# Kernel tuning notes

Hardware: AMD Instinct MI355X
Metric: run time of the kernel (lower is better)

Reference implementation:

```python
import jax, jax.numpy as jnp
import numpy as np

N = 50000      # total nodes across batch of graphs
E = 800000     # total directed edges (avg degree 16)
B = 64         # number of graphs
D = 128        # input_dim == hidden_dim
L = 4          # num_layers - 1 GIN layers
OUT = 10
BN_EPS = 1e-5


def setup_inputs() -> dict:
    key = jax.random.key(0)
    ks = jax.random.split(key, 12)
    s = 0.05
    return {
        "x": jax.random.normal(ks[0], (N, D), jnp.float32),
        "pi": jax.random.uniform(ks[1], (B, 25), jnp.float32),
        "eps": jnp.zeros((L,), jnp.float32),
        "mlp_w1": jax.random.normal(ks[2], (L, D, D), jnp.float32) * s,
        "mlp_b1": jnp.zeros((L, D), jnp.float32),
        "mlp_bn_g": jnp.ones((L, D), jnp.float32),
        "mlp_bn_b": jnp.zeros((L, D), jnp.float32),
        "mlp_w2": jax.random.normal(ks[3], (L, D, D), jnp.float32) * s,
        "mlp_b2": jnp.zeros((L, D), jnp.float32),
        "bn_g": jnp.ones((L, D), jnp.float32),
        "bn_b": jnp.zeros((L, D), jnp.float32),
        "attend_w": jax.random.normal(ks[4], (D * (L + 1), 1), jnp.float32) * s,
        "attend_b": jnp.zeros((1,), jnp.float32),
        "pi_w": jax.random.normal(ks[5], (25, 16), jnp.float32) * s,
        "pi_b": jnp.zeros((16,), jnp.float32),
        "out_w": jax.random.normal(ks[6], (D * (L + 1) + 16, OUT), jnp.float32) * s,
        "out_b": jnp.zeros((OUT,), jnp.float32),
        "edge_index": jax.random.randint(ks[7], (2, E), 0, N, dtype=jnp.int32),
        "graph_id": jnp.sort(jax.random.randint(ks[8], (N,), 0, B, dtype=jnp.int32)),
    }


def _bn(z, g, b):
    # BatchNorm1d in training mode over all nodes (axis 0)
    m = z.mean(axis=0)
    v = z.var(axis=0)
    return (z - m) * jax.lax.rsqrt(v + BN_EPS) * g + b


def reference(x, pi, eps, mlp_w1, mlp_b1, mlp_bn_g, mlp_bn_b, mlp_w2, mlp_b2,
              bn_g, bn_b, attend_w, attend_b, pi_w, pi_b, out_w, out_b,
              edge_index, graph_id):
    src, dst = edge_index[0], edge_index[1]
    h = x
    reps = [x]
    for l in range(L):
        # GIN sum aggregation (learn_eps=True: no self-loops in Adj)
        pooled = jax.ops.segment_sum(h[src], dst, num_segments=N)
        pooled = pooled + (1.0 + eps[l]) * h
        # 2-layer MLP: Linear -> BN -> ReLU -> Linear
        z = jax.nn.relu(_bn(pooled @ mlp_w1[l] + mlp_b1[l], mlp_bn_g[l], mlp_bn_b[l]))
        z = z @ mlp_w2[l] + mlp_b2[l]
        # outer BN + ReLU
        h = jax.nn.relu(_bn(z, bn_g[l], bn_b[l]))
        reps.append(h)
    hr = jnp.concatenate(reps, axis=1)               # [N, D*(L+1)]
    # per-graph attention softmax over nodes
    scores = (hr @ attend_w + attend_b)[:, 0]        # [N]
    smax = jax.ops.segment_max(scores, graph_id, num_segments=B)
    e = jnp.exp(scores - smax[graph_id])
    denom = jax.ops.segment_sum(e, graph_id, num_segments=B)
    coef = e / denom[graph_id]
    gemb = jax.ops.segment_sum(hr * coef[:, None], graph_id, num_segments=B)  # [B, D*(L+1)]
    # persistence-image branch (PI computed host-side; treated as input)
    pie = jax.nn.relu(pi @ pi_w + pi_b)              # [B, 16]
    feat = jnp.concatenate([gemb, pie], axis=1)      # [B, D*(L+1)+16]
    return feat @ out_w + out_b                      # [B, OUT]
```

## Files before the change

kernel.cpp:

```cpp
#include <hip/hip_runtime.h>
#include <hip/hip_bf16.h>

#define NN 50000
#define EE 800000
#define BBG 64
#define DD 128
#define LLAY 4
#define HRW 640
#define NOUT 10
#define NXCD 8
#define NBUCK 196
#define BUCKCAP 4608
#define EB 250
#define ECH 3200

typedef __hip_bfloat16 bf16;
typedef __attribute__((ext_vector_type(8))) short short8;
typedef __attribute__((ext_vector_type(4))) float f32x4;

__device__ __forceinline__ float b2f(bf16 v) { return __bfloat162float(v); }
__device__ __forceinline__ float bflo(unsigned u) { return __uint_as_float(u << 16); }
__device__ __forceinline__ float bfhi(unsigned u) { return __uint_as_float(u & 0xffff0000u); }
__device__ __forceinline__ unsigned short f2bs(float v) {
  bf16 h = __float2bfloat16(v);
  unsigned short r; __builtin_memcpy(&r, &h, 2); return r;
}
__device__ __forceinline__ int dtype_of(const void* __restrict__ bng) {
  return (*(const unsigned*)bng == 0x3F800000u) ? 1 : 0;
}
__device__ __forceinline__ float ldf(const void* __restrict__ p, long i, int dt) {
  return dt ? ((const float*)p)[i] : b2f(((const bf16*)p)[i]);
}

__device__ __forceinline__ int xccid() {
  unsigned v;
  asm("s_getreg_b32 %0, hwreg(HW_REG_XCC_ID)" : "=s"(v));
  return (int)(v & (NXCD - 1));
}

__device__ __forceinline__ void fadd_l2(float* p, float v) {
  asm volatile("global_atomic_add_f32 %0, %1, off" :: "v"(p), "v"(v) : "memory");
}

__device__ __forceinline__ int lower_bound_i(const int* __restrict__ a, int n, int key) {
  int lo = 0, hi = n;
  while (lo < hi) { int mid = (lo + hi) >> 1; if (a[mid] < key) lo = mid + 1; else hi = mid; }
// ... 1 lines not shown
}

__global__ __launch_bounds__(256) void gnn_init(const void* __restrict__ x,
                                                bf16* __restrict__ hrb,
                                                const void* __restrict__ w1,
                                                const void* __restrict__ w2,
                                                bf16* __restrict__ w1t,
                                                bf16* __restrict__ w2t,
                                                const void* __restrict__ aw,
                                                float* __restrict__ scores,
                                                const int* __restrict__ ei,
                                                int* __restrict__ bucketCnt,
                                                unsigned* __restrict__ bucketStore,
                                                const void* __restrict__ bng) {
  int dt = dtype_of(bng);
  int tid = threadIdx.x;
  if (blockIdx.x >= 3375) {
    int i = (blockIdx.x - 3375) * 256 + tid;
    int l = i >> 14, rem = i & 16383, n = rem >> 7, k = rem & 127;
    long src = (long)l * 16384 + k * 128 + n;
    w1t[i] = __float2bfloat16(ldf(w1, src, dt));
    w2t[i] = __float2bfloat16(ldf(w2, src, dt));
    return;
  }
  if (blockIdx.x >= 3125) {
    __shared__ int lcnt[NBUCK], gbase[NBUCK];
    int bb = blockIdx.x - 3125;
    int base = bb * ECH;
    if (tid < NBUCK) lcnt[tid] = 0;
    __syncthreads();
    #pragma unroll
    for (int j = 0; j < 13; j++) {
      int k = j * 256 + tid;
      if (k < ECH) {
        int dst = ei[EE + base + k];
        atomicAdd(&lcnt[dst >> 8], 1);
      }
    }
    __syncthreads();
    if (tid < NBUCK) {
      gbase[tid] = atomicAdd(&bucketCnt[tid * 16], lcnt[tid]);
      lcnt[tid] = 0;
    }
    __syncthreads();
    #pragma unroll
    for (int j = 0; j < 13; j++) {
      int k = j * 256 + tid;
      if (k < ECH) {
        int e = base + k;
        int src = ei[e];
        int dst = ei[EE + e];
        int b = dst >> 8;
        int r = atomicAdd(&lcnt[b], 1);
        bucketStore[b * BUCKCAP + gbase[b] + r] =
            (unsigned)src | ((unsigned)(dst & 255) << 16);
      }
    }
    return;
  }
  int n = blockIdx.x * 16 + (tid >> 4);
  int il = tid & 15;
  long base = (long)n * DD + il * 8;
  float v[8];
  if (dt) {
    float4 a0 = *(const float4*)((const float*)x + base);
    float4 a1 = *(const float4*)((const float*)x + base + 4);
    v[0] = a0.x; v[1] = a0.y; v[2] = a0.z; v[3] = a0.w;
    v[4] = a1.x; v[5] = a1.y; v[6] = a1.z; v[7] = a1.w;
  } else {
    uint4 u = *(const uint4*)((const bf16*)x + base);
// ... 27 lines not shown
    if (tid < s) buf[tid] += buf[tid + s];
    __syncthreads();
  }
  int start = buf[0];
  int sz = bucketCnt[b * 16];
  __syncthreads();
  cnt[tid] = 0;
  __syncthreads();
  for (int j = 0; j < 18; j++) {
    int k = j * 256 + tid;
    if (k < sz) atomicAdd(&cnt[bucketStore[b * BUCKCAP + k] >> 16], 1);
  }
  __syncthreads();
  int c = cnt[tid];
  buf[tid] = c;
  __syncthreads();
  for (int ofs = 1; ofs < 256; ofs <<= 1) {
    int t = (tid >= ofs) ? buf[tid - ofs] : 0;
    __syncthreads();
    buf[tid] += t;
    __syncthreads();
  }
  dbase[tid] = buf[tid] - c;
  int d = b * 256 + tid;
  if (d <= NN) rowstart[d] = start + buf[tid] - c;
  cnt[tid] = 0;
  __syncthreads();
  for (int j = 0; j < 18; j++) {
    int k = j * 256 + tid;
    if (k < sz) {
      unsigned v = bucketStore[b * BUCKCAP + k];
      int dlo = v >> 16;
      int r = atomicAdd(&cnt[dlo], 1);
      csr_src[start + dbase[dlo] + r] = (int)(v & 0xFFFFu) | ((dlo & 15) << 16);
    }
  }
}

__device__ __forceinline__ float2 statsum(const float* __restrict__ stat, int c) {
  float s = 0.f, q = 0.f;
  #pragma unroll
  for (int k = 0; k < 8; k++) { s += stat[k * 256 + c]; q += stat[k * 256 + 128 + c]; }
  return make_float2(s, q);
}

__device__ __forceinline__ void acc8(float* a, uint4 u) {
  a[0] += bflo(u.x); a[1] += bfhi(u.x);
  a[2] += bflo(u.y); a[3] += bfhi(u.y);
  a[4] += bflo(u.z); a[5] += bfhi(u.z);
  a[6] += bflo(u.w); a[7] += bfhi(u.w);
}

__device__ __forceinline__ void ldg16(const bf16* __restrict__ stripe, int idx, int j,
                                      int q, int il,
                                      uint4& u0, uint4& u1, uint4& u2, uint4& u3) {
  int s0 = __shfl(idx, j + q, 64) & 0xFFFF;
  int s1 = __shfl(idx, j + 4 + q, 64) & 0xFFFF;
  int s2 = __shfl(idx, j + 8 + q, 64) & 0xFFFF;
  int s3 = __shfl(idx, j + 12 + q, 64) & 0xFFFF;
  u0 = *(const uint4*)(stripe + (size_t)s0 * HRW + il * 8);
  u1 = *(const uint4*)(stripe + (size_t)s1 * HRW + il * 8);
  u2 = *(const uint4*)(stripe + (size_t)s2 * HRW + il * 8);
  u3 = *(const uint4*)(stripe + (size_t)s3 * HRW + il * 8);
}

__global__ __launch_bounds__(256) void gnn_gmg1(const bf16* __restrict__ hrb, int l,
                                                const int* __restrict__ rowstart,
                                                const int* __restrict__ csr_src,
                                                const void* __restrict__ eps,
                                                const bf16* __restrict__ Wt,
                                                const void* __restrict__ bias, int biasOfs,
                                                bf16* __restrict__ out,
                                                float* __restrict__ statOut,
                                                const void* __restrict__ bng) {
  int dt = dtype_of(bng);
  __shared__ __align__(16) unsigned ar[16][68];
  __shared__ int rs[17];
  __shared__ int qhead;
  int tid = threadIdx.x, lane = tid & 63;
  int w = tid >> 6;
  int q = lane >> 4, il = lane & 15;
  int r0 = blockIdx.x * 16;
  const bf16* stripe = hrb + l * DD;
  float s = 1.0f + ldf(eps, l, dt);
  if (tid < 17) rs[tid] = rowstart[r0 + tid];
  if (tid == 0) qhead = 0;
  __syncthreads();

  int i, start = 0, end = 0, idx = 0;
  {
    int v;
    if (lane == 0) v = atomicAdd(&qhead, 1);
    i = __shfl(v, 0, 64);
    if (i < 16) {
      start = rs[i]; end = rs[i + 1];
      idx = (start + lane < end) ? csr_src[start + lane] : 0;
    }
  }
  while (i < 16) {
    int i_nxt;
    {
      int v;
      if (lane == 0) v = atomicAdd(&qhead, 1);
      i_nxt = __shfl(v, 0, 64);
    }
    int start_n = 0, end_n = 0, idx_n = 0;
    if (i_nxt < 16) {
      start_n = rs[i_nxt]; end_n = rs[i_nxt + 1];
      idx_n = (start_n + lane < end_n) ? csr_src[start_n + lane] : 0;
    }

    float a[8] = {0.f, 0.f, 0.f, 0.f, 0.f, 0.f, 0.f, 0.f};
    if (q == 0) {
      uint4 u = *(const uint4*)(stripe + (size_t)(r0 + i) * HRW + il * 8);
      a[0] = s * bflo(u.x); a[1] = s * bfhi(u.x);
      a[2] = s * bflo(u.y); a[3] = s * bfhi(u.y);
      a[4] = s * bflo(u.z); a[5] = s * bfhi(u.z);
      a[6] = s * bflo(u.w); a[7] = s * bfhi(u.w);
    }
    int p = start;
    int m = end - p; if (m > 64) m = 64;
    for (;;) {
      int j = 0;
      if (m >= 16) {
        uint4 c0, c1, c2, c3;
        ldg16(stripe, idx, 0, q, il, c0, c1, c2, c3);
        for (j = 16; j + 16 <= m; j += 16) {
          uint4 n0, n1, n2, n3;
          ldg16(stripe, idx, j, q, il, n0, n1, n2, n3);
          acc8(a, c0); acc8(a, c1); acc8(a, c2); acc8(a, c3);
          c0 = n0; c1 = n1; c2 = n2; c3 = n3;
        }
        acc8(a, c0); acc8(a, c1); acc8(a, c2); acc8(a, c3);
      }
      for (; j + 8 <= m; j += 8) {
        int s0 = __shfl(idx, j + q, 64) & 0xFFFF;
        int s1 = __shfl(idx, j + 4 + q, 64) & 0xFFFF;
        uint4 u0 = *(const uint4*)(stripe + (size_t)s0 * HRW + il * 8);
        uint4 u1 = *(const uint4*)(stripe + (size_t)s1 * HRW + il * 8);
        acc8(a, u0); acc8(a, u1);
      }
      for (; j + 4 <= m; j += 4) {
        int s0 = __shfl(idx, j + q, 64) & 0xFFFF;
        uint4 u0 = *(const uint4*)(stripe + (size_t)s0 * HRW + il * 8);
        acc8(a, u0);
      }
      for (; j < m; j++) {
        int s0 = __shfl(idx, j, 64) & 0xFFFF;
        if (q == 0) {
          uint4 u0 = *(const uint4*)(stripe + (size_t)s0 * HRW + il * 8);
          acc8(a, u0);
        }
      }
      p += m;
      if (p >= end) break;
      m = end - p; if (m > 64) m = 64;
      idx = (p + lane < end) ? csr_src[p + lane] : 0;
    }
    #pragma unroll
    for (int k = 0; k < 8; k++) {
      a[k] += __shfl_xor(a[k], 16, 64);
      a[k] += __shfl_xor(a[k], 32, 64);
    }
    if (q == 0) {
      uint4 o;
      o.x = (unsigned)f2bs(a[0]) | ((unsigned)f2bs(a[1]) << 16);
      o.y = (unsigned)f2bs(a[2]) | ((unsigned)f2bs(a[3]) << 16);
      o.z = (unsigned)f2bs(a[4]) | ((unsigned)f2bs(a[5]) << 16);
      o.w = (unsigned)f2bs(a[6]) | ((unsigned)f2bs(a[7]) << 16);
      *(uint4*)&ar[i][il * 4] = o;
    }
    i = i_nxt; start = start_n; end = end_n; idx = idx_n;
  }
  __syncthreads();

  int xid = xccid();
  #pragma unroll
  for (int t = 0; t < 2; t++) {
    int ct = w + t * 4;
    f32x4 acc = (f32x4){0.f, 0.f, 0.f, 0.f};
    #pragma unroll
    for (int ch = 0; ch < 4; ch++) {
      int k0 = ch * 32 + q * 8;
      uint4 raw2 = *(const uint4*)&ar[il][ch * 16 + q * 4];
      short8 af;
      __builtin_memcpy(&af, &raw2, 16);
      short8 bfv = *(const short8*)(Wt + (ct * 16 + il) * DD + k0);
      acc = __builtin_amdgcn_mfma_f32_16x16x32_bf16(af, bfv, acc, 0, 0, 0);
    }
    int col = ct * 16 + il;
    float bv = ldf(bias, biasOfs + col, dt);
    float ss = 0.f, qq = 0.f;
    #pragma unroll
    for (int r = 0; r < 4; r++) {
      int row = r0 + q * 4 + r;
      float v = acc[r] + bv;
      out[(size_t)row * DD + col] = __float2bfloat16(v);
      ss += v; qq += v * v;
    }
    ss += __shfl_xor(ss, 16, 64);  ss += __shfl_xor(ss, 32, 64);
    qq += __shfl_xor(qq, 16, 64);  qq += __shfl_xor(qq, 32, 64);
    if (q == 0) {
      fadd_l2(&statOut[xid * 256 + col], ss);
      fadd_l2(&statOut[xid * 256 + 128 + col], qq);
    }
  }
}

__global__ __launch_bounds__(256) void gnn_mgemm(const bf16* __restrict__ Abf,
                                                 const bf16* __restrict__ Wt,
                                                 const void* __restrict__ bias, int biasOfs,
                                                 bf16* __restrict__ out,
                                                 const float* __restrict__ statIn,
                                                 const void* __restrict__ g,
                                                 const void* __restrict__ bb, int parOfs,
                                                 float* __restrict__ statOut,
                                                 const void* __restrict__ bng) {
  int dt = dtype_of(bng);
  __shared__ float scf[128], shf[128];
  __shared__ float redS[4][128], redQ[4][128];
// ... 57 lines not shown
    if (q == 0) { redS[w][col] = s; redQ[w][col] = qq; }
  }
  __syncthreads();
  int xid = xccid();
  if (tid < 128) {
    float v = redS[0][tid] + redS[1][tid] + redS[2][tid] + redS[3][tid];
    fadd_l2(&statOut[xid * 256 + tid], v);
  } else {
    int c = tid - 128;
    float v = redQ[0][c] + redQ[1][c] + redQ[2][c] + redQ[3][c];
    fadd_l2(&statOut[xid * 256 + 128 + c], v);
  }
}

__global__ __launch_bounds__(256) void gnn_bn_relu(const bf16* __restrict__ z2,
                                                   const float* __restrict__ stat,
                                                   const void* __restrict__ g,
                                                   const void* __restrict__ bb, int parOfs,
                                                   bf16* __restrict__ hrb, int stripe,
                                                   const void* __restrict__ aw,
                                                   float* __restrict__ scores,
                                                   const void* __restrict__ bng) {
  int dt = dtype_of(bng);
  __shared__ float scf[128], shf[128], awf[128];
  int tid = threadIdx.x;
  if (tid < 128) {
    const float invN = 1.0f / NN;
    float2 sq = statsum(stat, tid);
    float m = sq.x * invN;
    float rs = rsqrtf(sq.y * invN - m * m + 1e-5f);
    float gg = ldf(g, parOfs + tid, dt), bv = ldf(bb, parOfs + tid, dt);
    scf[tid] = rs * gg;
    shf[tid] = bv - m * rs * gg;
    awf[tid] = ldf(aw, stripe * DD + tid, dt);
  }
  __syncthreads();
  int n = blockIdx.x * 16 + (tid >> 4);
  int il = tid & 15;
  int c0 = il * 8;
  uint4 u = *(const uint4*)(z2 + (size_t)n * DD + c0);
  float v[8];
  v[0] = bflo(u.x); v[1] = bfhi(u.x); v[2] = bflo(u.y); v[3] = bfhi(u.y);
  v[4] = bflo(u.z); v[5] = bfhi(u.z); v[6] = bflo(u.w); v[7] = bfhi(u.w);
  float ss = 0.f;
  #pragma unroll
  for (int k = 0; k < 8; k++) {
    v[k] = fmaxf(v[k] * scf[c0 + k] + shf[c0 + k], 0.f);
    ss += v[k] * awf[c0 + k];
  }
  uint4 o;
  o.x = (unsigned)f2bs(v[0]) | ((unsigned)f2bs(v[1]) << 16);
  o.y = (unsigned)f2bs(v[2]) | ((unsigned)f2bs(v[3]) << 16);
  o.z = (unsigned)f2bs(v[4]) | ((unsigned)f2bs(v[5]) << 16);
  o.w = (unsigned)f2bs(v[6]) | ((unsigned)f2bs(v[7]) << 16);
  *(uint4*)(hrb + (size_t)n * HRW + stripe * DD + c0) = o;
  ss += __shfl_xor(ss, 1, 64); ss += __shfl_xor(ss, 2, 64);
  ss += __shfl_xor(ss, 4, 64); ss += __shfl_xor(ss, 8, 64);
  if (il == 0) scores[n] += ss;
}

__global__ __launch_bounds__(128) void gnn_gemb(const bf16* __restrict__ hrb,
                                                const float* __restrict__ scores,
                                                const int* __restrict__ gid,
                                                float* __restrict__ gembp) {
  int b = blockIdx.x / 10;
  int part = blockIdx.x % 10;
  int chunk = part >> 1;
  int half = part & 1;
  int tid = threadIdx.x;
  int start = lower_bound_i(gid, NN, b);
  int end = lower_bound_i(gid, NN, b + 1);
  __shared__ float red[128];
  float mx = -3.4e38f;
  for (int n = start + tid; n < end; n += 128) mx = fmaxf(mx, scores[n]);
  red[tid] = mx;
  __syncthreads();
  for (int s = 64; s > 0; s >>= 1) {
    if (tid < s) red[tid] = fmaxf(red[tid], red[tid + s]);
    __syncthreads();
  }
  float smax = red[0];
  __syncthreads();
  float sum = 0.f;
  for (int n = start + tid; n < end; n += 128) sum += __expf(scores[n] - smax);
  red[tid] = sum;
  __syncthreads();
  for (int s = 64; s > 0; s >>= 1) {
    if (tid < s) red[tid] += red[tid + s];
// ... 81 lines not shown
  const void* bng  = d_in[5];
  const void* bnb  = d_in[6];
  const void* w2   = d_in[7];
  const void* b2   = d_in[8];
  const void* obng = d_in[9];
  const void* obnb = d_in[10];
  const void* aw   = d_in[11];
  const void* piw  = d_in[13];
  const void* pib  = d_in[14];
  const void* ow   = d_in[15];
  const void* ob   = d_in[16];
  const int*  ei   = (const int*)d_in[17];
  const int*  gid  = (const int*)d_in[18];

  bf16*  hrb      = (bf16*)d_ws;
  bf16*  z1       = hrb + (size_t)NN * HRW;
  bf16*  z2       = z1 + (size_t)NN * DD;
  bf16*  w1t      = z2 + (size_t)NN * DD;
  bf16*  w2t      = w1t + LLAY * DD * DD;
  float* statbufs = (float*)(w2t + LLAY * DD * DD);
  int*   bucketCnt= (int*)(statbufs + 8 * 2048);
  size_t zeroBytes = (size_t)(8 * 2048 + NBUCK * 16) * 4;
  float* gembp    = (float*)(bucketCnt + NBUCK * 16);
  float* scores   = gembp + (size_t)16 * BBG * HRW;
  int*   rowstart = (int*)(scores + NN);
  unsigned* bucketStore = (unsigned*)(rowstart + NN + 1);
  int*   csr_src  = (int*)(bucketStore + (size_t)NBUCK * BUCKCAP);

  hipMemsetAsync(statbufs, 0, zeroBytes, stream);
  gnn_init<<<3631, 256, 0, stream>>>(x, hrb, w1, w2, w1t, w2t, aw, scores,
                                     ei, bucketCnt, bucketStore, bng);
  gnn_csr<<<NBUCK, 256, 0, stream>>>(bucketCnt, bucketStore, rowstart, csr_src);

  for (int l = 0; l < LLAY; l++) {
    float* statA = statbufs + (l * 2 + 0) * 2048;
    float* statB = statbufs + (l * 2 + 1) * 2048;
    gnn_gmg1<<<NN / 16, 256, 0, stream>>>(hrb, l, rowstart, csr_src, eps,
                                          w1t + l * DD * DD, b1, l * DD,
                                          z1, statA, bng);
    gnn_mgemm<<<782, 256, 0, stream>>>(z1, w2t + l * DD * DD, b2, l * DD,
                                       z2, statA, bng, bnb, l * DD,
                                       statB, bng);
    gnn_bn_relu<<<NN / 16, 256, 0, stream>>>(z2, statB, obng, obnb, l * DD,
                                             hrb, l + 1, aw, scores, bng);
  }

  gnn_gemb<<<BBG * 10, 128, 0, stream>>>(hrb, scores, gid, gembp);
  gnn_final<<<BBG, 64, 0, stream>>>(gembp, pi, piw, pib, ow, ob, d_out, bng);
}
```

Before: 523.6 us.

## Fuse per-layer kernels into one cooperative persistent kernel with grid syncs

Replaces the 14 per-layer and readout kernel launches with a single cooperative persistent kernel. It uses grid.sync between the gather+GEMM1, GEMM2, BN/ReLU, attention-pooling and final stages, and loops over tiles with a grid sized from occupancy. The aim is to remove launch overhead and inter-kernel gaps. In exchange it adds grid-wide barrier costs, possibly lower occupancy from the 4-blocks-per-CU launch bound, and extra shared memory per block. The old multi-kernel path stays as a fallback.

```diff
diff --git a/kernel.cpp b/kernel.cpp
--- a/kernel.cpp
+++ b/kernel.cpp
@@ -1,5 +1,8 @@
 #include <hip/hip_runtime.h>
 #include <hip/hip_bf16.h>
+#include <hip/hip_cooperative_groups.h>
+
+namespace cg = cooperative_groups;
 
 #define NN 50000
 #define EE 800000
@@ -208,6 +211,390 @@
   u3 = *(const uint4*)(stripe + (size_t)s3 * HRW + il * 8);
 }
 
+__device__ __forceinline__ void gather_tile(const bf16* __restrict__ stripe,
+                                            const int* __restrict__ csr_src,
+                                            const int* rs, int* qhead_p,
+                                            unsigned (*ar)[68],
+                                            int r0, float s, int lane, int q, int il) {
+  int i, rstart = 0, rend = 0, idx = 0;
+  {
+    int v;
+    if (lane == 0) v = atomicAdd(qhead_p, 1);
+    i = __shfl(v, 0, 64);
+    if (i < 16) {
+      rstart = rs[i]; rend = rs[i + 1];
+      idx = (rstart + lane < rend) ? csr_src[rstart + lane] : 0;
+    }
+  }
+  while (i < 16) {
+    int i_nxt;
+    {
+      int v;
+      if (lane == 0) v = atomicAdd(qhead_p, 1);
+      i_nxt = __shfl(v, 0, 64);
+    }
+    int start_n = 0, end_n = 0, idx_n = 0;
+    if (i_nxt < 16) {
+      start_n = rs[i_nxt]; end_n = rs[i_nxt + 1];
+      idx_n = (start_n + lane < end_n) ? csr_src[start_n + lane] : 0;
+    }
+
+    float av[8] = {0.f, 0.f, 0.f, 0.f, 0.f, 0.f, 0.f, 0.f};
+    if (q == 0) {
+      uint4 u = *(const uint4*)(stripe + (size_t)(r0 + i) * HRW + il * 8);
+      av[0] = s * bflo(u.x); av[1] = s * bfhi(u.x);
+      av[2] = s * bflo(u.y); av[3] = s * bfhi(u.y);
+      av[4] = s * bflo(u.z); av[5] = s * bfhi(u.z);
+      av[6] = s * bflo(u.w); av[7] = s * bfhi(u.w);
+    }
+    int p = rstart;
+    int m = rend - p; if (m > 64) m = 64;
+    for (;;) {
+      int j = 0;
+      if (m >= 16) {
+        uint4 c0v, c1v, c2v, c3v;
+        ldg16(stripe, idx, 0, q, il, c0v, c1v, c2v, c3v);
+        for (j = 16; j + 16 <= m; j += 16) {
+          uint4 n0, n1, n2, n3;
+          ldg16(stripe, idx, j, q, il, n0, n1, n2, n3);
+          acc8(av, c0v); acc8(av, c1v); acc8(av, c2v); acc8(av, c3v);
+          c0v = n0; c1v = n1; c2v = n2; c3v = n3;
+        }
+        acc8(av, c0v); acc8(av, c1v); acc8(av, c2v); acc8(av, c3v);
+      }
+      for (; j + 8 <= m; j += 8) {
+        int s0 = __shfl(idx, j + q, 64) & 0xFFFF;
+        int s1 = __shfl(idx, j + 4 + q, 64) & 0xFFFF;
+        uint4 u0 = *(const uint4*)(stripe + (size_t)s0 * HRW + il * 8);
+        uint4 u1 = *(const uint4*)(stripe + (size_t)s1 * HRW + il * 8);
+        acc8(av, u0); acc8(av, u1);
+      }
+      for (; j + 4 <= m; j += 4) {
+        int s0 = __shfl(idx, j + q, 64) & 0xFFFF;
+        uint4 u0 = *(const uint4*)(stripe + (size_t)s0 * HRW + il * 8);
+        acc8(av, u0);
+      }
+      for (; j < m; j++) {
+        int s0 = __shfl(idx, j, 64) & 0xFFFF;
+        if (q == 0) {
+          uint4 u0 = *(const uint4*)(stripe + (size_t)s0 * HRW + il * 8);
+          acc8(av, u0);
+        }
+      }
+      p += m;
+      if (p >= rend) break;
+      m = rend - p; if (m > 64) m = 64;
+      idx = (p + lane < rend) ? csr_src[p + lane] : 0;
+    }
+    #pragma unroll
+    for (int k = 0; k < 8; k++) {
+      av[k] += __shfl_xor(av[k], 16, 64);
+      av[k] += __shfl_xor(av[k], 32, 64);
+    }
+    if (q == 0) {
+      uint4 o;
+      o.x = (unsigned)f2bs(av[0]) | ((unsigned)f2bs(av[1]) << 16);
+      o.y = (unsigned)f2bs(av[2]) | ((unsigned)f2bs(av[3]) << 16);
+      o.z = (unsigned)f2bs(av[4]) | ((unsigned)f2bs(av[5]) << 16);
+      o.w = (unsigned)f2bs(av[6]) | ((unsigned)f2bs(av[7]) << 16);
+      *(uint4*)&ar[i][il * 4] = o;
+    }
+    i = i_nxt; rstart = start_n; rend = end_n; idx = idx_n;
+  }
+}
+
+struct MegaArgs {
+  bf16* hrb;
+  const int* rowstart;
+  const int* csr_src;
+  const void* eps;
+  const bf16* w1t;
+  const bf16* w2t;
+  const void* b1;
+  const void* b2;
+  const void* bng;
+  const void* bnb;
+  const void* obng;
+  const void* obnb;
+  const void* aw;
+  float* scores;
+  bf16* z1;
+  bf16* z2;
+  float* statbufs;
+  float* gembp;
+  const int* gid;
+  const void* pi;
+  const void* piw;
+  const void* pib;
+  const void* ow;
+  const void* ob;
+  void* out;
+};
+
+__global__ __launch_bounds__(256, 4) void gnn_mega(MegaArgs a) {
+  cg::grid_group grid = cg::this_grid();
+  int dt = dtype_of(a.bng);
+  int tid = threadIdx.x, lane = tid & 63, w = tid >> 6;
+  int q = lane >> 4, il = lane & 15;
+  int xid = xccid();
+
+  __shared__ __align__(16) unsigned ar[16][68];
+  __shared__ int rs[17];
+  __shared__ int qhead;
+  __shared__ float scf[128], shf[128], awf[128];
+  __shared__ float redS[4][128], redQ[4][128];
+  __shared__ float red[2][128];
+
+  for (int l = 0; l < LLAY; l++) {
+    float* statA = a.statbufs + (l * 2 + 0) * 2048;
+    float* statB = a.statbufs + (l * 2 + 1) * 2048;
+    const bf16* stripe = a.hrb + l * DD;
+    const bf16* Wt1 = a.w1t + l * DD * DD;
+    const bf16* Wt2 = a.w2t + l * DD * DD;
+    float s = 1.0f + ldf(a.eps, l, dt);
+
+    for (int tile = blockIdx.x; tile < NN / 16; tile += gridDim.x) {
+      int r0 = tile * 16;
+      if (tid < 17) rs[tid] = a.rowstart[r0 + tid];
+      if (tid == 0) qhead = 0;
+      __syncthreads();
+      gather_tile(stripe, a.csr_src, rs, &qhead, ar, r0, s, lane, q, il);
+      __syncthreads();
+      #pragma unroll
+      for (int t2 = 0; t2 < 2; t2++) {
+        int ct = w + t2 * 4;
+        f32x4 macc = (f32x4){0.f, 0.f, 0.f, 0.f};
+        #pragma unroll
+        for (int ch = 0; ch < 4; ch++) {
+          uint4 raw2 = *(const uint4*)&ar[il][ch * 16 + q * 4];
+          short8 af;
+          __builtin_memcpy(&af, &raw2, 16);
+          short8 bfv = *(const short8*)(Wt1 + (ct * 16 + il) * DD + ch * 32 + q * 8);
+          macc = __builtin_amdgcn_mfma_f32_16x16x32_bf16(af, bfv, macc, 0, 0, 0);
+        }
+        int col = ct * 16 + il;
+        float bv = ldf(a.b1, l * DD + col, dt);
+        float ss = 0.f, qq = 0.f;
+        #pragma unroll
+        for (int r = 0; r < 4; r++) {
+          int row = r0 + q * 4 + r;
+          float v = macc[r] + bv;
+          a.z1[(size_t)row * DD + col] = __float2bfloat16(v);
+          ss += v; qq += v * v;
+        }
+        ss += __shfl_xor(ss, 16, 64);  ss += __shfl_xor(ss, 32, 64);
+        qq += __shfl_xor(qq, 16, 64);  qq += __shfl_xor(qq, 32, 64);
+        if (q == 0) {
+          fadd_l2(&statA[xid * 256 + col], ss);
+          fadd_l2(&statA[xid * 256 + 128 + col], qq);
+        }
+      }
+      __syncthreads();
+    }
+    grid.sync();
+
+    if (tid < 128) {
+      const float invN = 1.0f / NN;
+      float2 sq = statsum(statA, tid);
+      float m = sq.x * invN;
+      float rsi = rsqrtf(sq.y * invN - m * m + 1e-5f);
+      float gg = ldf(a.bng, l * DD + tid, dt), bv = ldf(a.bnb, l * DD + tid, dt);
+      scf[tid] = rsi * gg;
+      shf[tid] = bv - m * rsi * gg;
+    }
+    __syncthreads();
+    for (int tile = blockIdx.x; tile < 782; tile += gridDim.x) {
+      int r0b = (tile * 4 + w) * 16;
+      int arow = r0b + il;
+      int arowc = (arow < NN) ? arow : (NN - 1);
+      f32x4 acc[8];
+      #pragma unroll
+      for (int i = 0; i < 8; i++) acc[i] = (f32x4){0.f, 0.f, 0.f, 0.f};
+      #pragma unroll
+      for (int ch = 0; ch < 4; ch++) {
+        int k0 = ch * 32 + q * 8;
+        uint4 raw = *(const uint4*)(a.z1 + (size_t)arowc * DD + k0);
+        float4 c0 = *(const float4*)(scf + k0);
+        float4 c1 = *(const float4*)(scf + k0 + 4);
+        float4 d0 = *(const float4*)(shf + k0);
+        float4 d1 = *(const float4*)(shf + k0 + 4);
+        short8 af;
+        af[0] = (short)f2bs(fmaxf(bflo(raw.x) * c0.x + d0.x, 0.f));
+        af[1] = (short)f2bs(fmaxf(bfhi(raw.x) * c0.y + d0.y, 0.f));
+        af[2] = (short)f2bs(fmaxf(bflo(raw.y) * c0.z + d0.z, 0.f));
+        af[3] = (short)f2bs(fmaxf(bfhi(raw.y) * c0.w + d0.w, 0.f));
+        af[4] = (short)f2bs(fmaxf(bflo(raw.z) * c1.x + d1.x, 0.f));
+        af[5] = (short)f2bs(fmaxf(bfhi(raw.z) * c1.y + d1.y, 0.f));
+        af[6] = (short)f2bs(fmaxf(bflo(raw.w) * c1.z + d1.z, 0.f));
+        af[7] = (short)f2bs(fmaxf(bfhi(raw.w) * c1.w + d1.w, 0.f));
+        #pragma unroll
+        for (int ct = 0; ct < 8; ct++) {
+          short8 bfv = *(const short8*)(Wt2 + (ct * 16 + il) * DD + k0);
+          acc[ct] = __builtin_amdgcn_mfma_f32_16x16x32_bf16(af, bfv, acc[ct], 0, 0, 0);
+        }
+      }
+      #pragma unroll
+      for (int ct = 0; ct < 8; ct++) {
+        int col = ct * 16 + il;
+        float bv = ldf(a.b2, l * DD + col, dt);
+        float sv = 0.f, qq = 0.f;
+        #pragma unroll
+        for (int r = 0; r < 4; r++) {
+          int row = r0b + q * 4 + r;
+          float v = acc[ct][r] + bv;
+          if (row < NN) {
+            a.z2[(size_t)row * DD + col] = __float2bfloat16(v);
+            sv += v; qq += v * v;
+          }
+        }
+        sv += __shfl_xor(sv, 16, 64);  sv += __shfl_xor(sv, 32, 64);
+        qq += __shfl_xor(qq, 16, 64);  qq += __shfl_xor(qq, 32, 64);
+        if (q == 0) { redS[w][col] = sv; redQ[w][col] = qq; }
+      }
+      __syncthreads();
+      if (tid < 128) {
+        float v = redS[0][tid] + redS[1][tid] + redS[2][tid] + redS[3][tid];
+        fadd_l2(&statB[xid * 256 + tid], v);
+      } else {
+        int c = tid - 128;
+        float v = redQ[0][c] + redQ[1][c] + redQ[2][c] + redQ[3][c];
+        fadd_l2(&statB[xid * 256 + 128 + c], v);
+      }
+      __syncthreads();
+    }
+    grid.sync();
+
+    if (tid < 128) {
+      const float invN = 1.0f / NN;
+      float2 sq = statsum(statB, tid);
+      float m = sq.x * invN;
+      float rsi = rsqrtf(sq.y * invN - m * m + 1e-5f);
+      float gg = ldf(a.obng, l * DD + tid, dt), bv = ldf(a.obnb, l * DD + tid, dt);
+      scf[tid] = rsi * gg;
+      shf[tid] = bv - m * rsi * gg;
+      awf[tid] = ldf(a.aw, (l + 1) * DD + tid, dt);
+    }
+    __syncthreads();
+    for (int tile = blockIdx.x; tile < NN / 16; tile += gridDim.x) {
+      int n = tile * 16 + (tid >> 4);
+      int c0 = il * 8;
+      uint4 u = *(const uint4*)(a.z2 + (size_t)n * DD + c0);
+      float v[8];
+      v[0] = bflo(u.x); v[1] = bfhi(u.x); v[2] = bflo(u.y); v[3] = bfhi(u.y);
+      v[4] = bflo(u.z); v[5] = bfhi(u.z); v[6] = bflo(u.w); v[7] = bfhi(u.w);
+      float ss = 0.f;
+      #pragma unroll
+      for (int k = 0; k < 8; k++) {
+        v[k] = fmaxf(v[k] * scf[c0 + k] + shf[c0 + k], 0.f);
+        ss += v[k] * awf[c0 + k];
+      }
+      uint4 o;
+      o.x = (unsigned)f2bs(v[0]) | ((unsigned)f2bs(v[1]) << 16);
+      o.y = (unsigned)f2bs(v[2]) | ((unsigned)f2bs(v[3]) << 16);
+      o.z = (unsigned)f2bs(v[4]) | ((unsigned)f2bs(v[5]) << 16);
+      o.w = (unsigned)f2bs(v[6]) | ((unsigned)f2bs(v[7]) << 16);
+      *(uint4*)(a.hrb + (size_t)n * HRW + (l + 1) * DD + c0) = o;
+      ss += __shfl_xor(ss, 1, 64); ss += __shfl_xor(ss, 2, 64);
+      ss += __shfl_xor(ss, 4, 64); ss += __shfl_xor(ss, 8, 64);
+      if (il == 0) a.scores[n] += ss;
+    }
+    grid.sync();
+  }
+
+  for (int pb = blockIdx.x; pb < 320; pb += gridDim.x) {
+    __syncthreads();
+    int t = tid & 127, hid = tid >> 7;
+    int part = pb * 2 + hid;
+    int b = part / 10;
+    int sub = part % 10;
+    int chunk = sub >> 1;
+    int shalf = sub & 1;
+    int start = lower_bound_i(a.gid, NN, b);
+    int end = lower_bound_i(a.gid, NN, b + 1);
+    float mx = -3.4e38f;
+    for (int n = start + t; n < end; n += 128) mx = fmaxf(mx, a.scores[n]);
+    red[hid][t] = mx;
+    __syncthreads();
+    for (int s = 64; s > 0; s >>= 1) {
+      if (t < s) red[hid][t] = fmaxf(red[hid][t], red[hid][t + s]);
+      __syncthreads();
+    }
+    float smax = red[hid][0];
+    __syncthreads();
+    float sum = 0.f;
+    for (int n = start + t; n < end; n += 128) sum += __expf(a.scores[n] - smax);
+    red[hid][t] = sum;
+    __syncthreads();
+    for (int s = 64; s > 0; s >>= 1) {
+      if (t < s) red[hid][t] += red[hid][t + s];
+      __syncthreads();
+    }
+    float denom = red[hid][0];
+    float inv = (denom > 0.f) ? 1.0f / denom : 0.f;
+    int cg2 = t & 15;
+    int sl = shalf * 8 + (t >> 4);
+    int c0 = chunk * 128 + cg2 * 8;
+    float acc[8] = {0.f, 0.f, 0.f, 0.f, 0.f, 0.f, 0.f, 0.f};
+    for (int n = start + sl; n < end; n += 16) {
+      float wgt = __expf(a.scores[n] - smax) * inv;
+      uint4 u = *(const uint4*)(a.hrb + (size_t)n * HRW + c0);
+      acc[0] = fmaf(bflo(u.x), wgt, acc[0]);
+      acc[1] = fmaf(bfhi(u.x), wgt, acc[1]);
+      acc[2] = fmaf(bflo(u.y), wgt, acc[2]);
+      acc[3] = fmaf(bfhi(u.y), wgt, acc[3]);
+      acc[4] = fmaf(bflo(u.z), wgt, acc[4]);
+      acc[5] = fmaf(bfhi(u.z), wgt, acc[5]);
+      acc[6] = fmaf(bflo(u.w), wgt, acc[6]);
+      acc[7] = fmaf(bfhi(u.w), wgt, acc[7]);
+    }
+    float* dst = a.gembp + ((size_t)sl * BBG + b) * HRW + c0;
+    *(float4*)dst = make_float4(acc[0], acc[1], acc[2], acc[3]);
+    *(float4*)(dst + 4) = make_float4(acc[4], acc[5], acc[6], acc[7]);
+  }
+  grid.sync();
+
+  for (int b = blockIdx.x; b < BBG; b += gridDim.x) {
+    if (tid < 64) {
+      int t = tid;
+      float pieval = 0.f;
+      if (t < 16) {
+        float sv = ldf(a.pib, t, dt);
+        for (int i = 0; i < 25; i++)
+          sv += ldf(a.pi, b * 25 + i, dt) * ldf(a.piw, i * 16 + t, dt);
+        pieval = fmaxf(sv, 0.f);
+      }
+      float fv[11];
+      #pragma unroll
+      for (int i = 0; i < 11; i++) {
+        int c = t + i * 64;
+        float f = 0.f;
+        if (c < HRW) {
+          #pragma unroll
+          for (int s2 = 0; s2 < 16; s2++) f += a.gembp[((size_t)s2 * BBG + b) * HRW + c];
+        } else if (c < HRW + 16) {
+          f = pieval;
+        }
+        fv[i] = f;
+      }
+      for (int o = 0; o < NOUT; o++) {
+        float sv = 0.f;
+        #pragma unroll
+        for (int i = 0; i < 11; i++) {
+          int c = t + i * 64;
+          if (c < HRW + 16) sv += fv[i] * ldf(a.ow, (long)c * NOUT + o, dt);
+        }
+        #pragma unroll
+        for (int m = 32; m > 0; m >>= 1) sv += __shfl_xor(sv, m, 64);
+        if (t == 0) {
+          float r = sv + ldf(a.ob, o, dt);
+          if (dt) ((float*)a.out)[b * NOUT + o] = r;
+          else ((bf16*)a.out)[b * NOUT + o] = __float2bfloat16(r);
+        }
+      }
+    }
+  }
+}
+
 __global__ __launch_bounds__(256) void gnn_gmg1(const bf16* __restrict__ hrb, int l,
                                                 const int* __restrict__ rowstart,
                                                 const int* __restrict__ csr_src,
@@ -230,94 +617,8 @@
   if (tid < 17) rs[tid] = rowstart[r0 + tid];
   if (tid == 0) qhead = 0;
   __syncthreads();
-
-  int i, start = 0, end = 0, idx = 0;
-  {
-    int v;
-    if (lane == 0) v = atomicAdd(&qhead, 1);
-    i = __shfl(v, 0, 64);
-    if (i < 16) {
-      start = rs[i]; end = rs[i + 1];
-      idx = (start + lane < end) ? csr_src[start + lane] : 0;
-    }
-  }
-  while (i < 16) {
-    int i_nxt;
-    {
-      int v;
-      if (lane == 0) v = atomicAdd(&qhead, 1);
-      i_nxt = __shfl(v, 0, 64);
-    }
-    int start_n = 0, end_n = 0, idx_n = 0;
-    if (i_nxt < 16) {
-      start_n = rs[i_nxt]; end_n = rs[i_nxt + 1];
-      idx_n = (start_n + lane < end_n) ? csr_src[start_n + lane] : 0;
-    }
-
-    float a[8] = {0.f, 0.f, 0.f, 0.f, 0.f, 0.f, 0.f, 0.f};
-    if (q == 0) {
-      uint4 u = *(const uint4*)(stripe + (size_t)(r0 + i) * HRW + il * 8);
-      a[0] = s * bflo(u.x); a[1] = s * bfhi(u.x);
-      a[2] = s * bflo(u.y); a[3] = s * bfhi(u.y);
-      a[4] = s * bflo(u.z); a[5] = s * bfhi(u.z);
-      a[6] = s * bflo(u.w); a[7] = s * bfhi(u.w);
-    }
-    int p = start;
-    int m = end - p; if (m > 64) m = 64;
-    for (;;) {
-      int j = 0;
-      if (m >= 16) {
-        uint4 c0, c1, c2, c3;
-        ldg16(stripe, idx, 0, q, il, c0, c1, c2, c3);
-        for (j = 16; j + 16 <= m; j += 16) {
-          uint4 n0, n1, n2, n3;
-          ldg16(stripe, idx, j, q, il, n0, n1, n2, n3);
-          acc8(a, c0); acc8(a, c1); acc8(a, c2); acc8(a, c3);
-          c0 = n0; c1 = n1; c2 = n2; c3 = n3;
-        }
-        acc8(a, c0); acc8(a, c1); acc8(a, c2); acc8(a, c3);
-      }
-      for (; j + 8 <= m; j += 8) {
-        int s0 = __shfl(idx, j + q, 64) & 0xFFFF;
-        int s1 = __shfl(idx, j + 4 + q, 64) & 0xFFFF;
-        uint4 u0 = *(const uint4*)(stripe + (size_t)s0 * HRW + il * 8);
-        uint4 u1 = *(const uint4*)(stripe + (size_t)s1 * HRW + il * 8);
-        acc8(a, u0); acc8(a, u1);
-      }
-      for (; j + 4 <= m; j += 4) {
-        int s0 = __shfl(idx, j + q, 64) & 0xFFFF;
-        uint4 u0 = *(const uint4*)(stripe + (size_t)s0 * HRW + il * 8);
-        acc8(a, u0);
-      }
-      for (; j < m; j++) {
-        int s0 = __shfl(idx, j, 64) & 0xFFFF;
-        if (q == 0) {
-          uint4 u0 = *(const uint4*)(stripe + (size_t)s0 * HRW + il * 8);
-          acc8(a, u0);
-        }
-      }
-      p += m;
-      if (p >= end) break;
-      m = end - p; if (m > 64) m = 64;
-      idx = (p + lane < end) ? csr_src[p + lane] : 0;
-    }
-    #pragma unroll
-    for (int k = 0; k < 8; k++) {
-      a[k] += __shfl_xor(a[k], 16, 64);
-      a[k] += __shfl_xor(a[k], 32, 64);
-    }
-    if (q == 0) {
-      uint4 o;
-      o.x = (unsigned)f2bs(a[0]) | ((unsigned)f2bs(a[1]) << 16);
-      o.y = (unsigned)f2bs(a[2]) | ((unsigned)f2bs(a[3]) << 16);
-      o.z = (unsigned)f2bs(a[4]) | ((unsigned)f2bs(a[5]) << 16);
-      o.w = (unsigned)f2bs(a[6]) | ((unsigned)f2bs(a[7]) << 16);
-      *(uint4*)&ar[i][il * 4] = o;
-    }
-    i = i_nxt; start = start_n; end = end_n; idx = idx_n;
-  }
-  __syncthreads();
-
+  gather_tile(stripe, csr_src, rs, &qhead, ar, r0, s, lane, q, il);
+  __syncthreads();
   int xid = xccid();
   #pragma unroll
   for (int t = 0; t < 2; t++) {
@@ -325,11 +626,10 @@
     f32x4 acc = (f32x4){0.f, 0.f, 0.f, 0.f};
     #pragma unroll
     for (int ch = 0; ch < 4; ch++) {
-      int k0 = ch * 32 + q * 8;
       uint4 raw2 = *(const uint4*)&ar[il][ch * 16 + q * 4];
       short8 af;
       __builtin_memcpy(&af, &raw2, 16);
-      short8 bfv = *(const short8*)(Wt + (ct * 16 + il) * DD + k0);
+      short8 bfv = *(const short8*)(Wt + (ct * 16 + il) * DD + ch * 32 + q * 8);
       acc = __builtin_amdgcn_mfma_f32_16x16x32_bf16(af, bfv, acc, 0, 0, 0);
     }
     int col = ct * 16 + il;
@@ -622,19 +922,57 @@
                                      ei, bucketCnt, bucketStore, bng);
   gnn_csr<<<NBUCK, 256, 0, stream>>>(bucketCnt, bucketStore, rowstart, csr_src);
 
-  for (int l = 0; l < LLAY; l++) {
-    float* statA = statbufs + (l * 2 + 0) * 2048;
-    float* statB = statbufs + (l * 2 + 1) * 2048;
-    gnn_gmg1<<<NN / 16, 256, 0, stream>>>(hrb, l, rowstart, csr_src, eps,
-                                          w1t + l * DD * DD, b1, l * DD,
-                                          z1, statA, bng);
-    gnn_mgemm<<<782, 256, 0, stream>>>(z1, w2t + l * DD * DD, b2, l * DD,
-                                       z2, statA, bng, bnb, l * DD,
-                                       statB, bng);
-    gnn_bn_relu<<<NN / 16, 256, 0, stream>>>(z2, statB, obng, obnb, l * DD,
-                                             hrb, l + 1, aw, scores, bng);
-  }
-
-  gnn_gemb<<<BBG * 10, 128, 0, stream>>>(hrb, scores, gid, gembp);
-  gnn_final<<<BBG, 64, 0, stream>>>(gembp, pi, piw, pib, ow, ob, d_out, bng);
-}
+  static int coopGrid = -2;
+  if (coopGrid == -2) {
+    int perCU = 0;
+    if (hipOccupancyMaxActiveBlocksPerMultiprocessor(&perCU, gnn_mega, 256, 0)
+            == hipSuccess && perCU > 0) {
+      int nCU = 256;
+      hipDeviceProp_t prop;
+      int dev = 0;
+      if (hipGetDevice(&dev) == hipSuccess &&
+          hipGetDeviceProperties(&prop, dev) == hipSuccess)
+        nCU = prop.multiProcessorCount;
+      long g = (long)perCU * nCU;
+      if (g > 3125) g = 3125;
+      coopGrid = (int)g;
+    } else {
+      coopGrid = -1;
+    }
+  }
+
+  bool coopOK = false;
+  if (coopGrid >= 64) {
+    MegaArgs ma;
+    ma.hrb = hrb; ma.rowstart = rowstart; ma.csr_src = csr_src;
+    ma.eps = eps; ma.w1t = w1t; ma.w2t = w2t;
+    ma.b1 = b1; ma.b2 = b2;
+    ma.bng = bng; ma.bnb = bnb; ma.obng = obng; ma.obnb = obnb;
+    ma.aw = aw; ma.scores = scores;
+    ma.z1 = z1; ma.z2 = z2; ma.statbufs = statbufs; ma.gembp = gembp;
+    ma.gid = gid; ma.pi = pi; ma.piw = piw; ma.pib = pib;
+    ma.ow = ow; ma.ob = ob; ma.out = d_out;
+    void* kargs[] = { &ma };
+    hipError_t le = hipLaunchCooperativeKernel(gnn_mega, dim3(coopGrid), dim3(256),
+                                               kargs, 0, stream);
+    coopOK = (le == hipSuccess);
+    if (!coopOK) coopGrid = -1;
+  }
+
+  if (!coopOK) {
+    for (int l = 0; l < LLAY; l++) {
+      float* statA = statbufs + (l * 2 + 0) * 2048;
+      float* statB = statbufs + (l * 2 + 1) * 2048;
+      gnn_gmg1<<<NN / 16, 256, 0, stream>>>(hrb, l, rowstart, csr_src, eps,
+                                            w1t + l * DD * DD, b1, l * DD,
+                                            z1, statA, bng);
+      gnn_mgemm<<<782, 256, 0, stream>>>(z1, w2t + l * DD * DD, b2, l * DD,
+                                         z2, statA, bng, bnb, l * DD,
+                                         statB, bng);
+      gnn_bn_relu<<<NN / 16, 256, 0, stream>>>(z2, statB, obng, obnb, l * DD,
+                                               hrb, l + 1, aw, scores, bng);
+    }
+    gnn_gemb<<<BBG * 10, 128, 0, stream>>>(hrb, scores, gid, gembp);
+    gnn_final<<<BBG, 64, 0, stream>>>(gembp, pi, piw, pib, ow, ob, d_out, bng);
+  }
+}
```

Result: slower. 1.533 ms (+192.8%).

## Fuse outer BN+ReLU into next layer's neighbor gather, reading compact z2

Applied to the files above, without the earlier changes.

For layers after the first, the gather kernel now reads raw z2 rows (stride 128) and applies the previous layer's outer BatchNorm and ReLU on the fly to each gathered neighbor. The self-row path writes the normalized h into the concatenated buffer and adds its attention score. This removes three separate bn_relu launches, and each gathered row now comes from a dense 128-wide array instead of a 640-wide strided one, which should help cache locality. The cost is that BN+ReLU is recomputed once per edge instead of once per node, adding ALU work in the gather loop. The csr_src packing of dst low bits is also dropped.

```diff
diff --git a/kernel.cpp b/kernel.cpp
--- a/kernel.cpp
+++ b/kernel.cpp
@@ -11,7 +11,6 @@
 #define NXCD 8
 #define NBUCK 196
 #define BUCKCAP 4608
-#define EB 250
 #define ECH 3200
 
 typedef __hip_bfloat16 bf16;
@@ -79,10 +78,7 @@
     #pragma unroll
     for (int j = 0; j < 13; j++) {
       int k = j * 256 + tid;
-      if (k < ECH) {
-        int dst = ei[EE + base + k];
-        atomicAdd(&lcnt[dst >> 8], 1);
-      }
+      if (k < ECH) atomicAdd(&lcnt[ei[EE + base + k] >> 8], 1);
     }
     __syncthreads();
     if (tid < NBUCK) {
@@ -176,7 +172,7 @@
       unsigned v = bucketStore[b * BUCKCAP + k];
       int dlo = v >> 16;
       int r = atomicAdd(&cnt[dlo], 1);
-      csr_src[start + dbase[dlo] + r] = (int)(v & 0xFFFFu) | ((dlo & 15) << 16);
+      csr_src[start + dbase[dlo] + r] = (int)(v & 0xFFFFu);
     }
   }
 }
@@ -188,30 +184,50 @@
   return make_float2(s, q);
 }
 
-__device__ __forceinline__ void acc8(float* a, uint4 u) {
-  a[0] += bflo(u.x); a[1] += bfhi(u.x);
-  a[2] += bflo(u.y); a[3] += bfhi(u.y);
-  a[4] += bflo(u.z); a[5] += bfhi(u.z);
-  a[6] += bflo(u.w); a[7] += bfhi(u.w);
-}
-
-__device__ __forceinline__ void ldg16(const bf16* __restrict__ stripe, int idx, int j,
-                                      int q, int il,
-                                      uint4& u0, uint4& u1, uint4& u2, uint4& u3) {
+template <bool L0>
+__device__ __forceinline__ void accT(float* a, uint4 u,
+                                     const float* sc, const float* sh) {
+  if (L0) {
+    a[0] += bflo(u.x); a[1] += bfhi(u.x);
+    a[2] += bflo(u.y); a[3] += bfhi(u.y);
+    a[4] += bflo(u.z); a[5] += bfhi(u.z);
+    a[6] += bflo(u.w); a[7] += bfhi(u.w);
+  } else {
+    a[0] += fmaxf(fmaf(bflo(u.x), sc[0], sh[0]), 0.f);
+    a[1] += fmaxf(fmaf(bfhi(u.x), sc[1], sh[1]), 0.f);
+    a[2] += fmaxf(fmaf(bflo(u.y), sc[2], sh[2]), 0.f);
+    a[3] += fmaxf(fmaf(bfhi(u.y), sc[3], sh[3]), 0.f);
+    a[4] += fmaxf(fmaf(bflo(u.z), sc[4], sh[4]), 0.f);
+    a[5] += fmaxf(fmaf(bfhi(u.z), sc[5], sh[5]), 0.f);
+    a[6] += fmaxf(fmaf(bflo(u.w), sc[6], sh[6]), 0.f);
+    a[7] += fmaxf(fmaf(bfhi(u.w), sc[7], sh[7]), 0.f);
+  }
+}
+
+__device__ __forceinline__ void ldg16s(const bf16* __restrict__ src, int sstride,
+                                       int idx, int j, int q, int il,
+                                       uint4& u0, uint4& u1, uint4& u2, uint4& u3) {
   int s0 = __shfl(idx, j + q, 64) & 0xFFFF;
   int s1 = __shfl(idx, j + 4 + q, 64) & 0xFFFF;
   int s2 = __shfl(idx, j + 8 + q, 64) & 0xFFFF;
   int s3 = __shfl(idx, j + 12 + q, 64) & 0xFFFF;
-  u0 = *(const uint4*)(stripe + (size_t)s0 * HRW + il * 8);
-  u1 = *(const uint4*)(stripe + (size_t)s1 * HRW + il * 8);
-  u2 = *(const uint4*)(stripe + (size_t)s2 * HRW + il * 8);
-  u3 = *(const uint4*)(stripe + (size_t)s3 * HRW + il * 8);
-}
-
-__global__ __launch_bounds__(256) void gnn_gmg1(const bf16* __restrict__ hrb, int l,
+  u0 = *(const uint4*)(src + (size_t)s0 * sstride + il * 8);
+  u1 = *(const uint4*)(src + (size_t)s1 * sstride + il * 8);
+  u2 = *(const uint4*)(src + (size_t)s2 * sstride + il * 8);
+  u3 = *(const uint4*)(src + (size_t)s3 * sstride + il * 8);
+}
+
+template <bool L0>
+__global__ __launch_bounds__(256) void gnn_gath(const bf16* __restrict__ src, int sstride,
                                                 const int* __restrict__ rowstart,
                                                 const int* __restrict__ csr_src,
-                                                const void* __restrict__ eps,
+                                                const void* __restrict__ eps, int l,
+                                                const float* __restrict__ statP,
+                                                const void* __restrict__ g,
+                                                const void* __restrict__ bb, int parOfs,
+                                                const void* __restrict__ aw,
+                                                bf16* __restrict__ hrb,
+                                                float* __restrict__ scores,
                                                 const bf16* __restrict__ Wt,
                                                 const void* __restrict__ bias, int biasOfs,
                                                 bf16* __restrict__ out,
@@ -221,24 +237,40 @@
   __shared__ __align__(16) unsigned ar[16][68];
   __shared__ int rs[17];
   __shared__ int qhead;
-  int tid = threadIdx.x, lane = tid & 63;
-  int w = tid >> 6;
+  __shared__ float scf[128], shf[128], awf[128];
+  int tid = threadIdx.x, lane = tid & 63, w = tid >> 6;
   int q = lane >> 4, il = lane & 15;
   int r0 = blockIdx.x * 16;
-  const bf16* stripe = hrb + l * DD;
-  float s = 1.0f + ldf(eps, l, dt);
+  float s1e = 1.0f + ldf(eps, l, dt);
+  if (!L0 && tid < 128) {
+    const float invN = 1.0f / NN;
+    float2 sq = statsum(statP, tid);
+    float m = sq.x * invN;
+    float rsi = rsqrtf(sq.y * invN - m * m + 1e-5f);
+    float gg = ldf(g, parOfs + tid, dt), bv = ldf(bb, parOfs + tid, dt);
+    scf[tid] = rsi * gg;
+    shf[tid] = bv - m * rsi * gg;
+    awf[tid] = ldf(aw, (long)l * DD + tid, dt);
+  }
   if (tid < 17) rs[tid] = rowstart[r0 + tid];
   if (tid == 0) qhead = 0;
   __syncthreads();
-
-  int i, start = 0, end = 0, idx = 0;
+  float sc[8], sh[8], aw8[8];
+  if (!L0) {
+    #pragma unroll
+    for (int k = 0; k < 8; k++) {
+      sc[k] = scf[il * 8 + k]; sh[k] = shf[il * 8 + k]; aw8[k] = awf[il * 8 + k];
+    }
+  }
+
+  int i, rstart = 0, rend = 0, idx = 0;
   {
     int v;
     if (lane == 0) v = atomicAdd(&qhead, 1);
     i = __shfl(v, 0, 64);
     if (i < 16) {
-      start = rs[i]; end = rs[i + 1];
-      idx = (start + lane < end) ? csr_src[start + lane] : 0;
+      rstart = rs[i]; rend = rs[i + 1];
+      idx = (rstart + lane < rend) ? csr_src[rstart + lane] : 0;
     }
   }
   while (i < 16) {
@@ -256,50 +288,76 @@
 
     float a[8] = {0.f, 0.f, 0.f, 0.f, 0.f, 0.f, 0.f, 0.f};
     if (q == 0) {
-      uint4 u = *(const uint4*)(stripe + (size_t)(r0 + i) * HRW + il * 8);
-      a[0] = s * bflo(u.x); a[1] = s * bfhi(u.x);
-      a[2] = s * bflo(u.y); a[3] = s * bfhi(u.y);
-      a[4] = s * bflo(u.z); a[5] = s * bfhi(u.z);
-      a[6] = s * bflo(u.w); a[7] = s * bfhi(u.w);
-    }
-    int p = start;
-    int m = end - p; if (m > 64) m = 64;
+      uint4 u = *(const uint4*)(src + (size_t)(r0 + i) * sstride + il * 8);
+      if (L0) {
+        a[0] = s1e * bflo(u.x); a[1] = s1e * bfhi(u.x);
+        a[2] = s1e * bflo(u.y); a[3] = s1e * bfhi(u.y);
+        a[4] = s1e * bflo(u.z); a[5] = s1e * bfhi(u.z);
+        a[6] = s1e * bflo(u.w); a[7] = s1e * bfhi(u.w);
+      } else {
+        float b0 = fmaxf(fmaf(bflo(u.x), sc[0], sh[0]), 0.f);
+        float b1 = fmaxf(fmaf(bfhi(u.x), sc[1], sh[1]), 0.f);
+        float b2 = fmaxf(fmaf(bflo(u.y), sc[2], sh[2]), 0.f);
+        float b3 = fmaxf(fmaf(bfhi(u.y), sc[3], sh[3]), 0.f);
+        float b4 = fmaxf(fmaf(bflo(u.z), sc[4], sh[4]), 0.f);
+        float b5 = fmaxf(fmaf(bfhi(u.z), sc[5], sh[5]), 0.f);
+        float b6 = fmaxf(fmaf(bflo(u.w), sc[6], sh[6]), 0.f);
+        float b7 = fmaxf(fmaf(bfhi(u.w), sc[7], sh[7]), 0.f);
+        uint4 o;
+        o.x = (unsigned)f2bs(b0) | ((unsigned)f2bs(b1) << 16);
+        o.y = (unsigned)f2bs(b2) | ((unsigned)f2bs(b3) << 16);
+        o.z = (unsigned)f2bs(b4) | ((unsigned)f2bs(b5) << 16);
+        o.w = (unsigned)f2bs(b6) | ((unsigned)f2bs(b7) << 16);
+        *(uint4*)(hrb + (size_t)(r0 + i) * HRW + (size_t)l * DD + il * 8) = o;
+        float sp = b0 * aw8[0] + b1 * aw8[1] + b2 * aw8[2] + b3 * aw8[3]
+                 + b4 * aw8[4] + b5 * aw8[5] + b6 * aw8[6] + b7 * aw8[7];
+        sp += __shfl_xor(sp, 1, 64); sp += __shfl_xor(sp, 2, 64);
+        sp += __shfl_xor(sp, 4, 64); sp += __shfl_xor(sp, 8, 64);
+        if (il == 0) scores[r0 + i] += sp;
+        a[0] = s1e * b0; a[1] = s1e * b1; a[2] = s1e * b2; a[3] = s1e * b3;
+        a[4] = s1e * b4; a[5] = s1e * b5; a[6] = s1e * b6; a[7] = s1e * b7;
+      }
+    }
+    int p = rstart;
+    int m = rend - p; if (m > 64) m = 64;
     for (;;) {
       int j = 0;
       if (m >= 16) {
         uint4 c0, c1, c2, c3;
-        ldg16(stripe, idx, 0, q, il, c0, c1, c2, c3);
+        ldg16s(src, sstride, idx, 0, q, il, c0, c1, c2, c3);
         for (j = 16; j + 16 <= m; j += 16) {
           uint4 n0, n1, n2, n3;
-          ldg16(stripe, idx, j, q, il, n0, n1, n2, n3);
-          acc8(a, c0); acc8(a, c1); acc8(a, c2); acc8(a, c3);
+          ldg16s(src, sstride, idx, j, q, il, n0, n1, n2, n3);
+          accT<L0>(a, c0, sc, sh); accT<L0>(a, c1, sc, sh);
+          accT<L0>(a, c2, sc, sh); accT<L0>(a, c3, sc, sh);
           c0 = n0; c1 = n1; c2 = n2; c3 = n3;
         }
-        acc8(a, c0); acc8(a, c1); acc8(a, c2); acc8(a, c3);
+        accT<L0>(a, c0, sc, sh); accT<L0>(a, c1, sc, sh);
+        accT<L0>(a, c2, sc, sh); accT<L0>(a, c3, sc, sh);
       }
       for (; j + 8 <= m; j += 8) {
         int s0 = __shfl(idx, j + q, 64) & 0xFFFF;
         int s1 = __shfl(idx, j + 4 + q, 64) & 0xFFFF;
-        uint4 u0 = *(const uint4*)(stripe + (size_t)s0 * HRW + il * 8);
-        uint4 u1 = *(const uint4*)(stripe + (size_t)s1 * HRW + il * 8);
-        acc8(a, u0); acc8(a, u1);
+        uint4 u0 = *(const uint4*)(src + (size_t)s0 * sstride + il * 8);
+        uint4 u1 = *(const uint4*)(src + (size_t)s1 * sstride + il * 8);
+        accT<L0>(a, u0, sc, sh); accT<L0>(a, u1, sc, sh);
       }
       for (; j + 4 <= m; j += 4) {
         int s0 = __shfl(idx, j + q, 64) & 0xFFFF;
-        uint4 u0 = *(const uint4*)(stripe + (size_t)s0 * HRW + il * 8);
-        acc8(a, u0);
+        uint4 u0 = *(const uint4*)(src + (size_t)s0 * sstride + il * 8);
+        accT<L0>(a, u0, sc, sh);
       }
       for (; j < m; j++) {
         int s0 = __shfl(idx, j, 64) & 0xFFFF;
         if (q == 0) {
-          uint4 u0 = *(const uint4*)(stripe + (size_t)s0 * HRW + il * 8);
-          acc8(a, u0);
+          uint4 u0 = *(const uint4*)(src + (size_t)s0 * sstride + il * 8);
+          accT<L0>(a, u0, sc, sh);
         }
       }
       p += m;
-      if (p >= end) break;
-      m = end - p; if (m > 64) m = 64;
-      idx = (p + lane < end) ? csr_src[p + lane] : 0;
+      if (p >= rend) break;
+      m = rend - p; if (m > 64) m = 64;
+      idx = (p + lane < rend) ? csr_src[p + lane] : 0;
     }
     #pragma unroll
     for (int k = 0; k < 8; k++) {
@@ -314,7 +372,7 @@
       o.w = (unsigned)f2bs(a[6]) | ((unsigned)f2bs(a[7]) << 16);
       *(uint4*)&ar[i][il * 4] = o;
     }
-    i = i_nxt; start = start_n; end = end_n; idx = idx_n;
+    i = i_nxt; rstart = start_n; rend = end_n; idx = idx_n;
   }
   __syncthreads();
 
@@ -325,11 +383,10 @@
     f32x4 acc = (f32x4){0.f, 0.f, 0.f, 0.f};
     #pragma unroll
     for (int ch = 0; ch < 4; ch++) {
-      int k0 = ch * 32 + q * 8;
       uint4 raw2 = *(const uint4*)&ar[il][ch * 16 + q * 4];
       short8 af;
       __builtin_memcpy(&af, &raw2, 16);
-      short8 bfv = *(const short8*)(Wt + (ct * 16 + il) * DD + k0);
+      short8 bfv = *(const short8*)(Wt + (ct * 16 + il) * DD + ch * 32 + q * 8);
       acc = __builtin_amdgcn_mfma_f32_16x16x32_bf16(af, bfv, acc, 0, 0, 0);
     }
     int col = ct * 16 + il;
@@ -453,7 +510,7 @@
     float gg = ldf(g, parOfs + tid, dt), bv = ldf(bb, parOfs + tid, dt);
     scf[tid] = rs * gg;
     shf[tid] = bv - m * rs * gg;
-    awf[tid] = ldf(aw, stripe * DD + tid, dt);
+    awf[tid] = ldf(aw, (long)stripe * DD + tid, dt);
   }
   __syncthreads();
   int n = blockIdx.x * 16 + (tid >> 4);
@@ -474,7 +531,7 @@
   o.y = (unsigned)f2bs(v[2]) | ((unsigned)f2bs(v[3]) << 16);
   o.z = (unsigned)f2bs(v[4]) | ((unsigned)f2bs(v[5]) << 16);
   o.w = (unsigned)f2bs(v[6]) | ((unsigned)f2bs(v[7]) << 16);
-  *(uint4*)(hrb + (size_t)n * HRW + stripe * DD + c0) = o;
+  *(uint4*)(hrb + (size_t)n * HRW + (size_t)stripe * DD + c0) = o;
   ss += __shfl_xor(ss, 1, 64); ss += __shfl_xor(ss, 2, 64);
   ss += __shfl_xor(ss, 4, 64); ss += __shfl_xor(ss, 8, 64);
   if (il == 0) scores[n] += ss;
@@ -625,16 +682,26 @@
   for (int l = 0; l < LLAY; l++) {
     float* statA = statbufs + (l * 2 + 0) * 2048;
     float* statB = statbufs + (l * 2 + 1) * 2048;
-    gnn_gmg1<<<NN / 16, 256, 0, stream>>>(hrb, l, rowstart, csr_src, eps,
-                                          w1t + l * DD * DD, b1, l * DD,
-                                          z1, statA, bng);
+    if (l == 0) {
+      gnn_gath<true><<<NN / 16, 256, 0, stream>>>(
+          hrb, HRW, rowstart, csr_src, eps, l,
+          statbufs, obng, obnb, 0, aw, hrb, scores,
+          w1t + l * DD * DD, b1, l * DD, z1, statA, bng);
+    } else {
+      const float* statP = statbufs + ((l - 1) * 2 + 1) * 2048;
+      gnn_gath<false><<<NN / 16, 256, 0, stream>>>(
+          z2, DD, rowstart, csr_src, eps, l,
+          statP, obng, obnb, (l - 1) * DD, aw, hrb, scores,
+          w1t + l * DD * DD, b1, l * DD, z1, statA, bng);
+    }
     gnn_mgemm<<<782, 256, 0, stream>>>(z1, w2t + l * DD * DD, b2, l * DD,
                                        z2, statA, bng, bnb, l * DD,
                                        statB, bng);
-    gnn_bn_relu<<<NN / 16, 256, 0, stream>>>(z2, statB, obng, obnb, l * DD,
-                                             hrb, l + 1, aw, scores, bng);
-  }
-
+  }
+
+  gnn_bn_relu<<<NN / 16, 256, 0, stream>>>(z2, statbufs + (3 * 2 + 1) * 2048,
+                                           obng, obnb, 3 * DD,
+                                           hrb, 4, aw, scores, bng);
   gnn_gemb<<<BBG * 10, 128, 0, stream>>>(hrb, scores, gid, gembp);
   gnn_final<<<BBG, 64, 0, stream>>>(gembp, pi, piw, pib, ow, ob, d_out, bng);
 }
```

Measured after the change: 617.8 us. 18.0% more time.
